# Kernel tuning notes

Measured on AMD Instinct MI355X. Metric: run time of the kernel, lower is better.

The kernel has to match this reference:

```python
import jax, jax.numpy as jnp
import numpy as np

N_NODES = 100000
N_EDGES = 1600000
NEG_SLOPE = 0.2  # PyG GATConv default


def _gat_layer(x, src, dst, W, a_src, a_dst, b, heads, concat):
    """One PyG-style GATConv (eval mode, self-loops already appended)."""
    N = x.shape[0]
    xp = (x @ W).reshape(N, heads, -1)                      # [N, H, C]
    al_s = jnp.einsum('nhc,hc->nh', xp, a_src)              # [N, H]
    al_d = jnp.einsum('nhc,hc->nh', xp, a_dst)              # [N, H]
    e = jax.nn.leaky_relu(al_s[src] + al_d[dst], NEG_SLOPE)  # [E, H]
    # numerically stable segment softmax over incoming edges of each dst
    m = jax.ops.segment_max(e, dst, num_segments=N)         # [N, H]
    ex = jnp.exp(e - m[dst])
    s = jax.ops.segment_sum(ex, dst, num_segments=N)
    alpha = ex / (s[dst] + 1e-16)                           # [E, H]
    out = jax.ops.segment_sum(xp[src] * alpha[:, :, None], dst, num_segments=N)  # [N, H, C]
    out = out.reshape(N, -1) if concat else out.mean(axis=1)
    return out + b


def setup_inputs() -> dict:
    key = jax.random.key(0)
    ks = jax.random.split(key, 16)
    H, C0 = 4, 32  # hidden layers: 4 heads x 32 = 128
    inp = {
        'x': jax.random.normal(ks[0], (N_NODES, 128), dtype=jnp.float32),
        'edge_index': jax.random.randint(ks[1], (2, N_EDGES), 0, N_NODES, dtype=jnp.int64),
        'W0': jax.random.normal(ks[2], (128, 128), dtype=jnp.float32) * 0.1,
        'a_src0': jax.random.normal(ks[3], (H, C0), dtype=jnp.float32) * 0.1,
        'a_dst0': jax.random.normal(ks[4], (H, C0), dtype=jnp.float32) * 0.1,
        'b0': jnp.zeros((128,), dtype=jnp.float32),
        'W1': jax.random.normal(ks[5], (128, 128), dtype=jnp.float32) * 0.1,
        'a_src1': jax.random.normal(ks[6], (H, C0), dtype=jnp.float32) * 0.1,
        'a_dst1': jax.random.normal(ks[7], (H, C0), dtype=jnp.float32) * 0.1,
        'b1': jnp.zeros((128,), dtype=jnp.float32),
        'W2': jax.random.normal(ks[8], (128, 64), dtype=jnp.float32) * 0.1,
        'a_src2': jax.random.normal(ks[9], (1, 64), dtype=jnp.float32) * 0.1,
        'a_dst2': jax.random.normal(ks[10], (1, 64), dtype=jnp.float32) * 0.1,
        'b2': jnp.zeros((64,), dtype=jnp.float32),
    }
    return inp


def reference(x, edge_index, W0, a_src0, a_dst0, b0, W1, a_src1, a_dst1, b1, W2, a_src2, a_dst2, b2):
    N = x.shape[0]
    loop = jnp.arange(N, dtype=edge_index.dtype)
    src = jnp.concatenate([edge_index[0], loop])  # add_self_loops=True
    dst = jnp.concatenate([edge_index[1], loop])
    h = _gat_layer(x, src, dst, W0, a_src0, a_dst0, b0, heads=4, concat=True)
    h = jax.nn.elu(h)
    h = _gat_layer(h, src, dst, W1, a_src1, a_dst1, b1, heads=4, concat=True)
    h = jax.nn.elu(h)
    out = _gat_layer(h, src, dst, W2, a_src2, a_dst2, b2, heads=1, concat=False)
    return out
```

## Files before the change

kernel.cpp:

```cpp
#include <hip/hip_runtime.h>
#include <math.h>


#define N_NODES 100000
#define NBUCK ((N_NODES + 255) / 256)

typedef __attribute__((ext_vector_type(4))) _Float16 half4;
typedef __attribute__((ext_vector_type(8))) _Float16 half8;
typedef __attribute__((ext_vector_type(4))) float f32x4;


__global__ __launch_bounds__(256) void k_bcount(const int* __restrict__ ei, int E, int ETOT,
                                                int* __restrict__ bucketCnt) {
    __shared__ int h[NBUCK];
    for (int b = threadIdx.x; b < NBUCK; b += 256) h[b] = 0;
    __syncthreads();
    const int base = blockIdx.x * 4096;
#pragma unroll
    for (int j = 0; j < 16; ++j) {
        int idx = base + j * 256 + threadIdx.x;
        if (idx < ETOT) {
            int dst = (idx < E) ? ei[E + idx] : (idx - E);
            atomicAdd(&h[dst >> 8], 1);
        }
    }
    __syncthreads();
    for (int b = threadIdx.x; b < NBUCK; b += 256)
        if (h[b]) atomicAdd(&bucketCnt[b], h[b]);
}

__global__ __launch_bounds__(256) void k_bscan(const int* __restrict__ bucketCnt,
                                               int* __restrict__ bstart,
                                               int* __restrict__ gcur, int ETOT) {
    __shared__ int lds[512];
    const int t = threadIdx.x;
    lds[t] = (t < NBUCK) ? bucketCnt[t] : 0;
    lds[t + 256] = (t + 256 < NBUCK) ? bucketCnt[t + 256] : 0;
    __syncthreads();
    for (int d = 1; d < 512; d <<= 1) {
        int v0 = (t >= d) ? lds[t - d] : 0;
        int v1 = (t + 256 >= d) ? lds[t + 256 - d] : 0;
        __syncthreads();
        lds[t] += v0;
        lds[t + 256] += v1;
        __syncthreads();
    }
    int e0 = (t == 0) ? 0 : lds[t - 1];
    int e1 = lds[t + 255];
    if (t < NBUCK)       { bstart[t] = e0;       gcur[t] = e0; }
    if (t + 256 < NBUCK) { bstart[t + 256] = e1; gcur[t + 256] = e1; }
    if (t == 0) bstart[NBUCK] = ETOT;
}

__global__ __launch_bounds__(256) void k_bplace(const int* __restrict__ ei, int E, int ETOT,
                                                int* __restrict__ gcur, int* __restrict__ tmp) {
    __shared__ int h[NBUCK];
    __shared__ int cur[NBUCK];
    for (int b = threadIdx.x; b < NBUCK; b += 256) h[b] = 0;
    __syncthreads();
    const int base = blockIdx.x * 4096;
    int pk[16], bk[16];
#pragma unroll
    for (int j = 0; j < 16; ++j) {
        int idx = base + j * 256 + threadIdx.x;
        bk[j] = -1;
        if (idx < ETOT) {
            int s, d;
            if (idx < E) { s = ei[idx]; d = ei[E + idx]; }
            else         { s = idx - E; d = idx - E; }
            bk[j] = d >> 8;
            pk[j] = s | ((d & 255) << 17);
            atomicAdd(&h[bk[j]], 1);
        }
    }
    __syncthreads();
    for (int b = threadIdx.x; b < NBUCK; b += 256)
        cur[b] = h[b] ? atomicAdd(&gcur[b], h[b]) : 0;
    __syncthreads();
#pragma unroll
    for (int j = 0; j < 16; ++j) {
        if (bk[j] >= 0) {
            int pos = atomicAdd(&cur[bk[j]], 1);
            tmp[pos] = pk[j];
        }
    }
}

__global__ __launch_bounds__(256) void k_bfinal(const int* __restrict__ tmp,
                                                const int* __restrict__ bstart,
                                                int* __restrict__ rowptr,
                                                int* __restrict__ ssrc, int N) {
    __shared__ int cnt[256];
    __shared__ int cur[256];
    const int t = threadIdx.x;
    const int b = blockIdx.x;
    const int s0 = bstart[b], s1 = bstart[b + 1];
    cnt[t] = 0;
    __syncthreads();
    for (int e = s0 + t; e < s1; e += 256)
        atomicAdd(&cnt[tmp[e] >> 17], 1);
    __syncthreads();
    int c0 = cnt[t];
    for (int d = 1; d < 256; d <<= 1) {
        int v = (t >= d) ? cnt[t - d] : 0;
        __syncthreads();
        cnt[t] += v;
        __syncthreads();
    }
    int excl = cnt[t] - c0;
    int node = b * 256 + t;
    if (node <= N) rowptr[node] = s0 + excl;
    cur[t] = excl;
    __syncthreads();
    for (int e = s0 + t; e < s1; e += 256) {
        int p = tmp[e];
        int pos = atomicAdd(&cur[p >> 17], 1);
        ssrc[s0 + pos] = p & 0x1FFFF;
    }
}

__global__ void k_wt3(const float* __restrict__ W0, const float* __restrict__ W1,
                      const float* __restrict__ W2, _Float16* __restrict__ wt0,
                      _Float16* __restrict__ wt1, _Float16* __restrict__ wt2) {
    int idx = blockIdx.x * 256 + threadIdx.x;
    if (idx < 16384) {
        int k = idx >> 7, n = idx & 127;
        wt0[n * 128 + k] = (_Float16)W0[idx];
    } else if (idx < 32768) {
        int i = idx - 16384;
        int k = i >> 7, n = i & 127;
        wt1[n * 128 + k] = (_Float16)W1[i];
    } else if (idx < 40960) {
        int i = idx - 32768;
        int k = i >> 6, n = i & 63;
        wt2[n * 128 + k] = (_Float16)W2[i];
    }
}

template <int OUT, int H, bool INF16>
__global__ __launch_bounds__(256) void k_gemm(const void* __restrict__ Xv_,
                                              const _Float16* __restrict__ Wt,
                                              const float* __restrict__ a_src,
                                              const float* __restrict__ a_dst,
                                              _Float16* __restrict__ XP,
                                              float* __restrict__ al_s,
                                              float* __restrict__ al_d, int N) {
    constexpr int NT = OUT / 16;
    constexpr int C = OUT / H;
    constexpr int LDH = 136;
    __shared__ _Float16 As[64 * LDH];
    __shared__ _Float16 Ws[OUT * LDH];
    const int tid = threadIdx.x;
    const int row0 = blockIdx.x * 64;

    for (int c = tid; c < OUT * 16; c += 256) {
        int r = c >> 4, kc = c & 15;
        *(half8*)&Ws[r * LDH + kc * 8] = *(const half8*)(Wt + r * 128 + kc * 8);
    }
    for (int c = tid; c < 64 * 16; c += 256) {
        int r = c >> 4, kc = c & 15;
        int grow = row0 + r;
        half8 hv;
        if (grow < N) {
            if constexpr (INF16) {
                hv = *(const half8*)((const _Float16*)Xv_ + (size_t)grow * 128 + kc * 8);
            } else {
                const float4* xr = (const float4*)((const float*)Xv_ + (size_t)grow * 128 + kc * 8);
                float4 x0 = xr[0], x1 = xr[1];
                hv[0] = (_Float16)x0.x; hv[1] = (_Float16)x0.y;
                hv[2] = (_Float16)x0.z; hv[3] = (_Float16)x0.w;
                hv[4] = (_Float16)x1.x; hv[5] = (_Float16)x1.y;
                hv[6] = (_Float16)x1.z; hv[7] = (_Float16)x1.w;
            }
        } else {
#pragma unroll
            for (int j = 0; j < 8; ++j) hv[j] = (_Float16)0.f;
        }
        *(half8*)&As[r * LDH + kc * 8] = hv;
    }
    __syncthreads();

    const int w = tid >> 6;
    const int l = tid & 63;
    const int lm = l & 15;
    const int lk = l >> 4;

    f32x4 acc[NT];
#pragma unroll
    for (int nt = 0; nt < NT; ++nt) acc[nt] = {0.f, 0.f, 0.f, 0.f};

#pragma unroll
    for (int ks = 0; ks < 4; ++ks) {
        half8 av = *(const half8*)&As[(w * 16 + lm) * LDH + ks * 32 + lk * 8];
#pragma unroll
        for (int nt = 0; nt < NT; ++nt) {
            half8 bv = *(const half8*)&Ws[(nt * 16 + lm) * LDH + ks * 32 + lk * 8];
            acc[nt] = __builtin_amdgcn_mfma_f32_16x16x32_f16(av, bv, acc[nt], 0, 0, 0);
        }
    }

    float avs[NT], avd[NT];
#pragma unroll
    for (int nt = 0; nt < NT; ++nt) {
        avs[nt] = a_src[nt * 16 + lm];
        avd[nt] = a_dst[nt * 16 + lm];
    }

#pragma unroll
    for (int r = 0; r < 4; ++r) {
        int grow = row0 + w * 16 + lk * 4 + r;
        bool ok = grow < N;
#pragma unroll
        for (int nt = 0; nt < NT; ++nt)
            if (ok) XP[(size_t)grow * OUT + nt * 16 + lm] = (_Float16)acc[nt][r];

        float ps[H], pd[H];
#pragma unroll
        for (int h = 0; h < H; ++h) { ps[h] = 0.f; pd[h] = 0.f; }
#pragma unroll
        for (int nt = 0; nt < NT; ++nt) {
            int h = (nt * 16) / C;
            ps[h] += acc[nt][r] * avs[nt];
            pd[h] += acc[nt][r] * avd[nt];
        }
#pragma unroll
        for (int h = 0; h < H; ++h) {
#pragma unroll
            for (int o = 8; o >= 1; o >>= 1) {
                ps[h] += __shfl_xor(ps[h], o);
                pd[h] += __shfl_xor(pd[h], o);
            }
        }
        if (ok && lm == 0) {
#pragma unroll
            for (int h = 0; h < H; ++h) {
                al_s[(size_t)grow * H + h] = ps[h];
                al_d[(size_t)grow * H + h] = pd[h];
            }
        }
    }
}

template <int OUT, int H, bool ELU, bool OUTF16>
__global__ __launch_bounds__(256) void k_agg(const _Float16* __restrict__ xp,
                                             const float* __restrict__ al_s,
                                             const float* __restrict__ al_d,
                                             const int* __restrict__ rowptr,
                                             const int* __restrict__ ssrc,
                                             const float* __restrict__ bias,
                                             void* __restrict__ out_, int N) {
    constexpr int C = OUT / H;
    constexpr int CPL = OUT / 16;
    const int wid = threadIdx.x >> 6;
    const int lane = threadIdx.x & 63;
    const int qid = lane >> 4;
    const int l4 = lane & 15;
    const int node = blockIdx.x * 4 + wid;
    if (node >= N) return;
    const int rs = rowptr[node];
    const int re = rowptr[node + 1];

    const int c0 = l4 * CPL;
    const int hd = c0 / C;
    const float adh = al_d[(size_t)node * H + hd];

    float ssum = 0.f;
    float acc[CPL];
#pragma unroll
    for (int j = 0; j < CPL; ++j) acc[j] = 0.f;

    auto edge = [&](int idx) {
        int s = ssrc[idx];
        float e = al_s[(size_t)s * H + hd] + adh;
        e = e > 0.f ? e : 0.2f * e;
        float a = __expf(e);
        ssum += a;
        if constexpr (CPL == 8) {
            half8 v = *(const half8*)(xp + (size_t)s * OUT + c0);
#pragma unroll
            for (int j = 0; j < 8; ++j) acc[j] += a * (float)v[j];
        } else {
            half4 v = *(const half4*)(xp + (size_t)s * OUT + c0);
#pragma unroll
            for (int j = 0; j < 4; ++j) acc[j] += a * (float)v[j];
        }
    };

    int i = rs;
    for (; i + 16 <= re; i += 16) {
        edge(i + qid); edge(i + qid + 4); edge(i + qid + 8); edge(i + qid + 12);
    }
    for (; i + 8 <= re; i += 8) {
        edge(i + qid); edge(i + qid + 4);
    }
    for (; i + qid < re; i += 4) {
        edge(i + qid);
    }

    ssum += __shfl_xor(ssum, 16);
    ssum += __shfl_xor(ssum, 32);
#pragma unroll
    for (int j = 0; j < CPL; ++j) {
        acc[j] += __shfl_xor(acc[j], 16);
        acc[j] += __shfl_xor(acc[j], 32);
    }

    if (qid == 0) {
        float inv = 1.f / (ssum + 1e-16f);
        float o[CPL];
#pragma unroll
        for (int j = 0; j < CPL; ++j) {
            o[j] = acc[j] * inv + bias[c0 + j];
            if constexpr (ELU) o[j] = o[j] > 0.f ? o[j] : (__expf(o[j]) - 1.f);
        }
        if constexpr (OUTF16) {
            _Float16* op = (_Float16*)out_ + (size_t)node * OUT + c0;
            if constexpr (CPL == 8) {
                half8 hv;
#pragma unroll
                for (int j = 0; j < 8; ++j) hv[j] = (_Float16)o[j];
                *(half8*)op = hv;
            } else {
                half4 hv;
#pragma unroll
                for (int j = 0; j < 4; ++j) hv[j] = (_Float16)o[j];
                *(half4*)op = hv;
            }
        } else {
            float* op = (float*)out_ + (size_t)node * OUT + c0;
            if constexpr (CPL == 8) {
                *(float4*)op = make_float4(o[0], o[1], o[2], o[3]);
                *(float4*)(op + 4) = make_float4(o[4], o[5], o[6], o[7]);
            } else {
                *(float4*)op = make_float4(o[0], o[1], o[2], o[3]);
            }
        }
    }
}


extern "C" void kernel_launch(void* const* d_in, const int* in_sizes, int n_in,
                              void* d_out, int out_size, void* d_ws, size_t ws_size,
                              hipStream_t stream) {
    const int N = N_NODES;
    const float* x     = (const float*)d_in[0];
    const int*   ei    = (const int*)d_in[1];
    const float* W0    = (const float*)d_in[2];
    const float* as0   = (const float*)d_in[3];
    const float* ad0   = (const float*)d_in[4];
    const float* b0    = (const float*)d_in[5];
    const float* W1    = (const float*)d_in[6];
    const float* as1   = (const float*)d_in[7];
    const float* ad1   = (const float*)d_in[8];
    const float* b1    = (const float*)d_in[9];
    const float* W2    = (const float*)d_in[10];
    const float* as2   = (const float*)d_in[11];
    const float* ad2   = (const float*)d_in[12];
    const float* b2    = (const float*)d_in[13];
    float* out = (float*)d_out;

    const int E = in_sizes[1] / 2;
    const int ETOT = E + N;

    char* p = (char*)d_ws;
    auto alloc = [&](size_t bytes) {
        void* r = (void*)p;
        p += (bytes + 255) & ~(size_t)255;
        return r;
    };
    _Float16* xp    = (_Float16*)alloc((size_t)N * 128 * 2);
    _Float16* hbuf  = (_Float16*)alloc((size_t)N * 128 * 2);
    float* als      = (float*)alloc((size_t)N * 4 * 4);
    float* ald      = (float*)alloc((size_t)N * 4 * 4);
    int*   rowptr   = (int*)alloc((size_t)(N + 1) * 4);
    int*   ssrc     = (int*)alloc((size_t)ETOT * 4);
    int*   tmp      = (int*)alloc((size_t)ETOT * 4);
    int*   bucketCnt= (int*)alloc((size_t)NBUCK * 4);
    int*   bstart   = (int*)alloc((size_t)(NBUCK + 1) * 4);
    int*   gcur     = (int*)alloc((size_t)NBUCK * 4);
    _Float16* wt0   = (_Float16*)alloc((size_t)128 * 128 * 2);
    _Float16* wt1   = (_Float16*)alloc((size_t)128 * 128 * 2);
    _Float16* wt2   = (_Float16*)alloc((size_t)128 * 64 * 2);

    k_wt3<<<160, 256, 0, stream>>>(W0, W1, W2, wt0, wt1, wt2);

    const int PB = (ETOT + 4095) / 4096;
    hipMemsetAsync(bucketCnt, 0, (size_t)NBUCK * 4, stream);
    k_bcount<<<PB, 256, 0, stream>>>(ei, E, ETOT, bucketCnt);
    k_bscan<<<1, 256, 0, stream>>>(bucketCnt, bstart, gcur, ETOT);
    k_bplace<<<PB, 256, 0, stream>>>(ei, E, ETOT, gcur, tmp);
    k_bfinal<<<NBUCK, 256, 0, stream>>>(tmp, bstart, rowptr, ssrc, N);

    const int gGemm = (N + 63) / 64;
    const int gAgg  = (N + 3) / 4;

    k_gemm<128, 4, false><<<gGemm, 256, 0, stream>>>(x, wt0, as0, ad0, xp, als, ald, N);
    k_agg<128, 4, true, true><<<gAgg, 256, 0, stream>>>(xp, als, ald, rowptr, ssrc, b0, hbuf, N);

    k_gemm<128, 4, true><<<gGemm, 256, 0, stream>>>(hbuf, wt1, as1, ad1, xp, als, ald, N);
    k_agg<128, 4, true, true><<<gAgg, 256, 0, stream>>>(xp, als, ald, rowptr, ssrc, b1, hbuf, N);

    k_gemm<64, 1, true><<<gGemm, 256, 0, stream>>>(hbuf, wt2, as2, ad2, xp, als, ald, N);
    k_agg<64, 1, false, false><<<gAgg, 256, 0, stream>>>(xp, als, ald, rowptr, ssrc, b2, out, N);
}
```

Baseline: 322.0 us.

## Precompute per-edge attention exponentials in separate kernel and use fma_mix accumulation

```diff
diff --git a/kernel.cpp b/kernel.cpp
--- a/kernel.cpp
+++ b/kernel.cpp
@@ -8,6 +8,11 @@
 typedef __attribute__((ext_vector_type(4))) _Float16 half4;
 typedef __attribute__((ext_vector_type(8))) _Float16 half8;
 typedef __attribute__((ext_vector_type(4))) float f32x4;
+
+__device__ inline void fmamix2(float& alo, float& ahi, float s, unsigned u) {
+    asm("v_fma_mix_f32 %0, %1, %2, %0 op_sel_hi:[0,1,0]" : "+v"(alo) : "v"(s), "v"(u));
+    asm("v_fma_mix_f32 %0, %1, %2, %0 op_sel:[0,1,0] op_sel_hi:[0,1,0]" : "+v"(ahi) : "v"(s), "v"(u));
+}
 
 
 __global__ __launch_bounds__(256) void k_bcount(const int* __restrict__ ei, int E, int ETOT,
@@ -89,7 +94,8 @@
 __global__ __launch_bounds__(256) void k_bfinal(const int* __restrict__ tmp,
                                                 const int* __restrict__ bstart,
                                                 int* __restrict__ rowptr,
-                                                int* __restrict__ ssrc, int N) {
+                                                int* __restrict__ ssrc,
+                                                int* __restrict__ sdst, int N) {
     __shared__ int cnt[256];
     __shared__ int cur[256];
     const int t = threadIdx.x;
@@ -116,6 +122,7 @@
         int p = tmp[e];
         int pos = atomicAdd(&cur[p >> 17], 1);
         ssrc[s0 + pos] = p & 0x1FFFF;
+        sdst[s0 + pos] = (b << 8) | (p >> 17);
     }
 }
 
@@ -241,10 +248,33 @@
     }
 }
 
+template <int H>
+__global__ __launch_bounds__(256) void k_edge(const int* __restrict__ ssrc,
+                                              const int* __restrict__ sdst,
+                                              const float* __restrict__ al_s,
+                                              const float* __restrict__ al_d,
+                                              float* __restrict__ alpha, int ETOT) {
+    int idx = blockIdx.x * 256 + threadIdx.x;
+    if (idx >= ETOT) return;
+    int s = ssrc[idx], d = sdst[idx];
+    if constexpr (H == 4) {
+        float4 as = ((const float4*)al_s)[s];
+        float4 ad = ((const float4*)al_d)[d];
+        float e0 = as.x + ad.x; e0 = e0 > 0.f ? e0 : 0.2f * e0;
+        float e1 = as.y + ad.y; e1 = e1 > 0.f ? e1 : 0.2f * e1;
+        float e2 = as.z + ad.z; e2 = e2 > 0.f ? e2 : 0.2f * e2;
+        float e3 = as.w + ad.w; e3 = e3 > 0.f ? e3 : 0.2f * e3;
+        ((float4*)alpha)[idx] = make_float4(__expf(e0), __expf(e1), __expf(e2), __expf(e3));
+    } else {
+        float e = al_s[s] + al_d[d];
+        e = e > 0.f ? e : 0.2f * e;
+        alpha[idx] = __expf(e);
+    }
+}
+
 template <int OUT, int H, bool ELU, bool OUTF16>
 __global__ __launch_bounds__(256) void k_agg(const _Float16* __restrict__ xp,
-                                             const float* __restrict__ al_s,
-                                             const float* __restrict__ al_d,
+                                             const float* __restrict__ alpha,
                                              const int* __restrict__ rowptr,
                                              const int* __restrict__ ssrc,
                                              const float* __restrict__ bias,
@@ -262,7 +292,6 @@
 
     const int c0 = l4 * CPL;
     const int hd = c0 / C;
-    const float adh = al_d[(size_t)node * H + hd];
 
     float ssum = 0.f;
     float acc[CPL];
@@ -271,18 +300,19 @@
 
     auto edge = [&](int idx) {
         int s = ssrc[idx];
-        float e = al_s[(size_t)s * H + hd] + adh;
-        e = e > 0.f ? e : 0.2f * e;
-        float a = __expf(e);
+        float a = alpha[(unsigned)idx * H + hd];
         ssum += a;
+        unsigned off = (unsigned)s * OUT + c0;
         if constexpr (CPL == 8) {
-            half8 v = *(const half8*)(xp + (size_t)s * OUT + c0);
-#pragma unroll
-            for (int j = 0; j < 8; ++j) acc[j] += a * (float)v[j];
+            uint4 u = *(const uint4*)(xp + off);
+            fmamix2(acc[0], acc[1], a, u.x);
+            fmamix2(acc[2], acc[3], a, u.y);
+            fmamix2(acc[4], acc[5], a, u.z);
+            fmamix2(acc[6], acc[7], a, u.w);
         } else {
-            half4 v = *(const half4*)(xp + (size_t)s * OUT + c0);
-#pragma unroll
-            for (int j = 0; j < 4; ++j) acc[j] += a * (float)v[j];
+            uint2 u = *(const uint2*)(xp + off);
+            fmamix2(acc[0], acc[1], a, u.x);
+            fmamix2(acc[2], acc[3], a, u.y);
         }
     };
 
@@ -374,7 +404,9 @@
     float* ald      = (float*)alloc((size_t)N * 4 * 4);
     int*   rowptr   = (int*)alloc((size_t)(N + 1) * 4);
     int*   ssrc     = (int*)alloc((size_t)ETOT * 4);
-    int*   tmp      = (int*)alloc((size_t)ETOT * 4);
+    int*   sdst     = (int*)alloc((size_t)ETOT * 4);
+    float* alpha    = (float*)alloc((size_t)ETOT * 4 * 4);
+    int*   tmp      = (int*)alpha;
     int*   bucketCnt= (int*)alloc((size_t)NBUCK * 4);
     int*   bstart   = (int*)alloc((size_t)(NBUCK + 1) * 4);
     int*   gcur     = (int*)alloc((size_t)NBUCK * 4);
@@ -389,17 +421,21 @@
     k_bcount<<<PB, 256, 0, stream>>>(ei, E, ETOT, bucketCnt);
     k_bscan<<<1, 256, 0, stream>>>(bucketCnt, bstart, gcur, ETOT);
     k_bplace<<<PB, 256, 0, stream>>>(ei, E, ETOT, gcur, tmp);
-    k_bfinal<<<NBUCK, 256, 0, stream>>>(tmp, bstart, rowptr, ssrc, N);
+    k_bfinal<<<NBUCK, 256, 0, stream>>>(tmp, bstart, rowptr, ssrc, sdst, N);
 
     const int gGemm = (N + 63) / 64;
     const int gAgg  = (N + 3) / 4;
+    const int gEdge = (ETOT + 255) / 256;
 
     k_gemm<128, 4, false><<<gGemm, 256, 0, stream>>>(x, wt0, as0, ad0, xp, als, ald, N);
-    k_agg<128, 4, true, true><<<gAgg, 256, 0, stream>>>(xp, als, ald, rowptr, ssrc, b0, hbuf, N);
+    k_edge<4><<<gEdge, 256, 0, stream>>>(ssrc, sdst, als, ald, alpha, ETOT);
+    k_agg<128, 4, true, true><<<gAgg, 256, 0, stream>>>(xp, alpha, rowptr, ssrc, b0, hbuf, N);
 
     k_gemm<128, 4, true><<<gGemm, 256, 0, stream>>>(hbuf, wt1, as1, ad1, xp, als, ald, N);
-    k_agg<128, 4, true, true><<<gAgg, 256, 0, stream>>>(xp, als, ald, rowptr, ssrc, b1, hbuf, N);
+    k_edge<4><<<gEdge, 256, 0, stream>>>(ssrc, sdst, als, ald, alpha, ETOT);
+    k_agg<128, 4, true, true><<<gAgg, 256, 0, stream>>>(xp, alpha, rowptr, ssrc, b1, hbuf, N);
 
     k_gemm<64, 1, true><<<gGemm, 256, 0, stream>>>(hbuf, wt2, as2, ad2, xp, als, ald, N);
-    k_agg<64, 1, false, false><<<gAgg, 256, 0, stream>>>(xp, als, ald, rowptr, ssrc, b2, out, N);
-}
+    k_edge<1><<<gEdge, 256, 0, stream>>>(ssrc, sdst, als, ald, alpha, ETOT);
+    k_agg<64, 1, false, false><<<gAgg, 256, 0, stream>>>(xp, alpha, rowptr, ssrc, b2, out, N);
+}
```

New measurement: 343.7 us. 6.8% more time.
